# Performance work log

Measured on AMD Instinct MI355X. Metric: run time of the kernel, lower is better.

Reference implementation:

```python
import jax, jax.numpy as jnp
import numpy as np

EPS_BN = 1e-5
EPS_W = 1e-8


def setup_inputs() -> dict:
    key = jax.random.key(0)
    ks = jax.random.split(key, 6)
    B, N, S, D1, D2 = 8, 8192, 2048, 128, 256
    Cin = D1 + D2  # 384
    return {
        "points_position": jax.random.normal(ks[0], (B, 3, N), jnp.float32),
        "sampled_points_position": jax.random.normal(ks[1], (B, 3, S), jnp.float32),
        "skip_points_feature": jax.random.normal(ks[2], (B, D1, N), jnp.float32),
        "sampled_points_feature": jax.random.normal(ks[3], (B, D2, S), jnp.float32),
        "W1": jax.random.normal(ks[4], (256, Cin), jnp.float32) * 0.05,
        "b1": jnp.zeros((256,), jnp.float32),
        "g1": jnp.ones((256,), jnp.float32),
        "beta1": jnp.zeros((256,), jnp.float32),
        "W2": jax.random.normal(ks[5], (128, 256), jnp.float32) * 0.05,
        "b2": jnp.zeros((128,), jnp.float32),
        "g2": jnp.ones((128,), jnp.float32),
        "beta2": jnp.zeros((128,), jnp.float32),
    }


def _bn_relu(x, g, b):
    # train-mode BatchNorm1d over (batch, points) per channel, x: [B,N,C]
    mean = jnp.mean(x, axis=(0, 1), keepdims=True)
    var = jnp.mean(jnp.square(x - mean), axis=(0, 1), keepdims=True)  # biased var
    return jax.nn.relu((x - mean) * jax.lax.rsqrt(var + EPS_BN) * g + b)


def reference(points_position, sampled_points_position, skip_points_feature,
              sampled_points_feature, W1, b1, g1, beta1, W2, b2, g2, beta2):
    pos = points_position.transpose(0, 2, 1)            # [B,N,3]
    spos = sampled_points_position.transpose(0, 2, 1)   # [B,S,3]
    sfeat = sampled_points_feature.transpose(0, 2, 1)   # [B,S,D2]

    # squared pairwise distance [B,N,S]
    d = (jnp.sum(pos * pos, axis=-1, keepdims=True)
         - 2.0 * jnp.einsum("bnc,bsc->bns", pos, spos)
         + jnp.sum(spos * spos, axis=-1)[:, None, :])

    # 3 nearest neighbors (smallest distances)
    neg_d3, idx = jax.lax.top_k(-d, 3)                  # [B,N,3]
    d3 = -neg_d3
    w = 1.0 / (d3 + EPS_W)
    w = w / jnp.sum(w, axis=-1, keepdims=True)          # [B,N,3]

    gathered = jax.vmap(lambda f, i: f[i])(sfeat, idx)  # [B,N,3,D2]
    interp = jnp.einsum("bnk,bnkd->bnd", w, gathered)   # [B,N,D2]

    feat = jnp.concatenate([skip_points_feature.transpose(0, 2, 1), interp], axis=-1)  # [B,N,D1+D2]

    h = _bn_relu(jnp.einsum("bnc,oc->bno", feat, W1) + b1, g1, beta1)  # [B,N,256]
    h = _bn_relu(jnp.einsum("bnc,oc->bno", h, W2) + b2, g2, beta2)     # [B,N,128]
    return h.transpose(0, 2, 1)                          # [B,128,N]
```

## Files before the change

kernel.cpp:

```cpp
#include <hip/hip_runtime.h>

constexpr int BATCH = 8;
constexpr int NPT   = 8192;
constexpr int NSMP  = 2048;
constexpr int D1C   = 128;
constexpr int D2C   = 256;
constexpr int CIN   = 384;
constexpr int C1    = 256;
constexpr int C2    = 128;
constexpr int BN_TOTAL = BATCH * NPT;

constexpr int BM = 128, BK = 32;
constexpr int NRB = BN_TOTAL / BM;

typedef __bf16 bf16x8 __attribute__((ext_vector_type(8)));
typedef short  s16x8  __attribute__((ext_vector_type(8)));
typedef float  f32x4  __attribute__((ext_vector_type(4)));
typedef unsigned short u16x4 __attribute__((ext_vector_type(4)));

__device__ __forceinline__ unsigned short f2bf(float x) {
  unsigned u = __builtin_bit_cast(unsigned, x);
  u += 0x7fffu + ((u >> 16) & 1u);
  return (unsigned short)(u >> 16);
}
__device__ __forceinline__ float bf2f(unsigned short h) {
  return __builtin_bit_cast(float, (unsigned)h << 16);
}

__device__ __forceinline__ void gld_lds16(const void* g, void* l) {
  __builtin_amdgcn_global_load_lds(
      (const __attribute__((address_space(1))) void*)g,
      (__attribute__((address_space(3))) void*)l, 16, 0, 0);
}

constexpr int PT_T = (NSMP / 32) * (D2C / 32) * BATCH;
constexpr int PT_S = (NPT / 32) * (D1C / 32) * BATCH;
constexpr int PT_M = (C1 * CIN + 255) / 256;

__global__ __launch_bounds__(256) void prep_all(
    const float* __restrict__ sfeat, float* __restrict__ sfeatT,
    const float* __restrict__ skip, unsigned short* __restrict__ featB,
    const float* __restrict__ spos, float* __restrict__ sposI,
    float4* __restrict__ qs4,
    const float* __restrict__ W1, unsigned short* __restrict__ W1h,
    const float* __restrict__ W2, unsigned short* __restrict__ W2h,
    float* __restrict__ stats) {
  __shared__ float tile[32][33];
  int bid = blockIdx.x, tid = threadIdx.x;
  int tx = tid & 31, ty = tid >> 5;
  if (bid < PT_T) {
    int z = bid >> 9;
    int r = bid & 511;
    int c0 = (r & 63) * 32;
    int r0 = (r >> 6) * 32;
    const float* inb = sfeat + (size_t)z * D2C * NSMP;
    float* outb = sfeatT + (size_t)z * NSMP * D2C;
#pragma unroll
    for (int i = 0; i < 32; i += 8)
      tile[ty + i][tx] = inb[(size_t)(r0 + ty + i) * NSMP + c0 + tx];
    __syncthreads();
#pragma unroll
    for (int i = 0; i < 32; i += 8)
      outb[(size_t)(c0 + ty + i) * D2C + r0 + tx] = tile[tx][ty + i];
  } else if (bid < PT_T + PT_S) {
    int id = bid - PT_T;
    int z = id >> 10;
    int r = id & 1023;
    int n0 = (r & 255) * 32;
    int d0 = (r >> 8) * 32;
#pragma unroll
    for (int i = 0; i < 32; i += 8)
      tile[ty + i][tx] = skip[((size_t)z * D1C + d0 + ty + i) * NPT + n0 + tx];
    __syncthreads();
#pragma unroll
    for (int i = 0; i < 32; i += 8) {
      int n = n0 + ty + i;
      featB[((size_t)z * NPT + n) * CIN + d0 + tx] = f2bf(tile[tx][ty + i]);
    }
  } else {
    int g = (bid - PT_T - PT_S) * 256 + tid;
    if (g < 768) stats[g] = 0.f;
    if (g < C1 * CIN) W1h[g] = f2bf(W1[g]);
    if (g < C2 * C1)  W2h[g] = f2bf(W2[g]);
    if (g < BATCH * NSMP) {
      int b = g >> 11, s = g & (NSMP - 1);
      const float* sp = spos + (size_t)b * 3 * NSMP;
      float x = sp[s], y = sp[NSMP + s], z = sp[2 * NSMP + s];
      sposI[(size_t)g * 3 + 0] = x;
      sposI[(size_t)g * 3 + 1] = y;
      sposI[(size_t)g * 3 + 2] = z;
      qs4[g] = make_float4(-2.f * x, -2.f * y, -2.f * z,
                           fmaf(x, x, fmaf(y, y, z * z)));
    }
  }
}

constexpr int KWAVES = 8;
constexpr int SEGK = NSMP / KWAVES;
constexpr int PPB  = 128;

__device__ __forceinline__ void ins_med3(float kf, float& k0, float& k1,
                                         float& k2, float& k3) {
  float o0 = k0, o1 = k1, o2 = k2;
  k0 = fminf(kf, o0);
  k1 = __builtin_amdgcn_fmed3f(kf, o0, o1);
  k2 = __builtin_amdgcn_fmed3f(kf, o1, o2);
  k3 = __builtin_amdgcn_fmed3f(kf, o2, k3);
}

__device__ __forceinline__ bool dless(double d, int i, double D, int I) {
  return d < D || (d == D && i < I);
}
__device__ __forceinline__ void dins3(double d, int i,
                                      double& b0, double& b1, double& b2,
                                      int& i0, int& i1, int& i2) {
  if (dless(d, i, b2, i2)) {
    if (dless(d, i, b1, i1)) {
      b2 = b1; i2 = i1;
      if (dless(d, i, b0, i0)) { b1 = b0; i1 = i0; b0 = d; i0 = i; }
      else                     { b1 = d; i1 = i; }
    } else { b2 = d; i2 = i; }
  }
}

__global__ __launch_bounds__(512, 4) void knn_all(
    const float* __restrict__ pos,
    const float4* __restrict__ qs4g,
    const float* __restrict__ sposI,
    const float* __restrict__ sfeatT,
    unsigned short* __restrict__ featB) {
  __shared__ __align__(16) unsigned char smem[NSMP * 16];
  float4* qs  = (float4*)smem;
  float*  mkf = (float*)smem;
#define MKF(w, sl, m, l) mkf[(w) * 1024 + ((sl) * 2 + (m)) * 64 + (l)]
  __shared__ int   il[PPB][3];
  __shared__ float wl[PPB][3];
  __shared__ int   fl[PPB];
  __shared__ int   fcnt;

  int tid = threadIdx.x;
  int wave = tid >> 6, lane = tid & 63;
  int blk = blockIdx.x;
  int b = blk & 7;
  int n0 = (blk >> 3) * PPB;

  if (tid == 0) fcnt = 0;

  const float* pb = pos + (size_t)b * 3 * NPT;
  float px[2], py[2], pz[2], pp[2];
#pragma unroll
  for (int m = 0; m < 2; m++) {
    int n = n0 + (m << 6) + lane;
    px[m] = pb[n]; py[m] = pb[NPT + n]; pz[m] = pb[2 * NPT + n];
    pp[m] = fmaf(px[m], px[m], fmaf(py[m], py[m], pz[m] * pz[m]));
  }

  const float INF = __builtin_inff();
  float k0[2], k1[2], k2[2], k3[2];
#pragma unroll
  for (int m = 0; m < 2; m++) { k0[m] = INF; k1[m] = INF; k2[m] = INF; k3[m] = INF; }

  int s0 = wave * SEGK;
  const float4* qsrc = qs4g + (size_t)b * NSMP;
#pragma unroll
  for (int r = 0; r < 4; r++)
    gld_lds16(&qsrc[s0 + r * 64 + lane], &qs[s0 + r * 64]);
  __syncthreads();

#define KSTEP2(Q, SS)                                                        \
  {                                                                          \
    _Pragma("unroll")                                                        \
    for (int m_ = 0; m_ < 2; m_++) {                                         \
      float tt = (Q).w + pp[m_];       \
      float d_ = fmaf(px[m_], (Q).x,                                         \
                      fmaf(py[m_], (Q).y, fmaf(pz[m_], (Q).z, tt)));         \
      unsigned ki_ = (__builtin_bit_cast(unsigned, d_) & 0xFFFFF800u) |      \
                     (unsigned)(SS);                                         \
      ins_med3(__builtin_bit_cast(float, ki_), k0[m_], k1[m_], k2[m_], k3[m_]); \
    }                                                                        \
  }

  for (int t = 0; t < SEGK; t += 8) {
    float4 qv[8];
#pragma unroll
    for (int u = 0; u < 8; u++) qv[u] = qs[s0 + t + u];
#pragma unroll
    for (int u = 0; u < 8; u++) KSTEP2(qv[u], s0 + t + u)
  }
#undef KSTEP2

#pragma unroll
  for (int m = 0; m < 2; m++) {
    MKF(wave, 0, m, lane) = k0[m];
    MKF(wave, 1, m, lane) = k1[m];
    MKF(wave, 2, m, lane) = k2[m];
    MKF(wave, 3, m, lane) = k3[m];
  }
  __syncthreads();

  if (tid < PPB) {
    int pm = tid >> 6, pl = tid & 63;
    float K0 = INF, K1 = INF, K2 = INF, K3 = INF;
#pragma unroll
    for (int w = 0; w < KWAVES; w++)
#pragma unroll
      for (int sl = 0; sl < 4; sl++)
        ins_med3(MKF(w, sl, pm, pl), K0, K1, K2, K3);

    int I0 = (int)(__builtin_bit_cast(unsigned, K0) & 0x7FFu);
    int I1 = (int)(__builtin_bit_cast(unsigned, K1) & 0x7FFu);
    int I2 = (int)(__builtin_bit_cast(unsigned, K2) & 0x7FFu);
    float d2m = __builtin_bit_cast(float, __builtin_bit_cast(unsigned, K2) & 0xFFFFF800u);
    float d3m = __builtin_bit_cast(float, __builtin_bit_cast(unsigned, K3) & 0xFFFFF800u);
    bool flag = (d3m - d2m) < 2e-3f * fmaxf(d3m, 0.f) + 1e-5f;
    if (flag) {
      int slot = atomicAdd(&fcnt, 1);
      fl[slot] = tid;
    }
    int n = n0 + tid;
    const float* q = sposI + (size_t)b * 3 * NSMP;
    double pxd = (double)pb[n], pyd = (double)pb[NPT + n], pzd = (double)pb[2 * NPT + n];
    double dd[3]; int II[3] = {I0, I1, I2};
#pragma unroll
    for (int k = 0; k < 3; k++) {
      double dx = pxd - (double)q[3 * II[k]];
      double dy = pyd - (double)q[3 * II[k] + 1];
      double dz = pzd - (double)q[3 * II[k] + 2];
      dd[k] = dx * dx + dy * dy + dz * dz;
    }
    double w0 = 1.0 / (dd[0] + 1e-8);
    double w1 = 1.0 / (dd[1] + 1e-8);
    double w2 = 1.0 / (dd[2] + 1e-8);
    double inv = 1.0 / (w0 + w1 + w2);
    il[tid][0] = I0; il[tid][1] = I1; il[tid][2] = I2;
    wl[tid][0] = (float)(w0 * inv);
    wl[tid][1] = (float)(w1 * inv);
    wl[tid][2] = (float)(w2 * inv);
  }
  __syncthreads();

  int fc = fcnt;
  for (int t = wave; t < fc; t += KWAVES) {
    int P = fl[t];
    int n = n0 + P;
    double pxd = (double)pb[n], pyd = (double)pb[NPT + n], pzd = (double)pb[2 * NPT + n];
    const float* q = sposI + (size_t)b * 3 * NSMP;
    double b0 = 1e300, b1 = 1e300, b2 = 1e300;
    int i0 = 0x7FFFFFFF, i1 = 0x7FFFFFFF, i2 = 0x7FFFFFFF;
    for (int s = lane; s < NSMP; s += 64) {
      double dx = pxd - (double)q[3 * s];
      double dy = pyd - (double)q[3 * s + 1];
      double dz = pzd - (double)q[3 * s + 2];
      double d = dx * dx + dy * dy + dz * dz;
      dins3(d, s, b0, b1, b2, i0, i1, i2);
    }
#pragma unroll
    for (int m = 1; m < 64; m <<= 1) {
      double o0 = __shfl_xor(b0, m, 64), o1 = __shfl_xor(b1, m, 64), o2 = __shfl_xor(b2, m, 64);
      int    j0 = __shfl_xor(i0, m, 64), j1 = __shfl_xor(i1, m, 64), j2 = __shfl_xor(i2, m, 64);
      dins3(o0, j0, b0, b1, b2, i0, i1, i2);
      dins3(o1, j1, b0, b1, b2, i0, i1, i2);
      dins3(o2, j2, b0, b1, b2, i0, i1, i2);
    }
    if (lane == 0) {
      double w0 = 1.0 / (b0 + 1e-8);
      double w1 = 1.0 / (b1 + 1e-8);
      double w2 = 1.0 / (b2 + 1e-8);
      double inv = 1.0 / (w0 + w1 + w2);
      il[P][0] = i0; il[P][1] = i1; il[P][2] = i2;
      wl[P][0] = (float)(w0 * inv);
      wl[P][1] = (float)(w1 * inv);
      wl[P][2] = (float)(w2 * inv);
    }
  }
  __syncthreads();

  const float* base = sfeatT + (size_t)b * NSMP * D2C;
  for (int i = 0; i < 16; i++) {
    int P = (wave << 4) + i;
    int i0 = il[P][0], i1 = il[P][1], i2 = il[P][2];
    float w0 = wl[P][0], w1 = wl[P][1], w2 = wl[P][2];
    float4 v0 = *(const float4*)&base[(size_t)i0 * D2C + (lane << 2)];
    float4 v1 = *(const float4*)&base[(size_t)i1 * D2C + (lane << 2)];
    float4 v2 = *(const float4*)&base[(size_t)i2 * D2C + (lane << 2)];
    u16x4 o;
    o[0] = f2bf(w0 * v0.x + w1 * v1.x + w2 * v2.x);
    o[1] = f2bf(w0 * v0.y + w1 * v1.y + w2 * v2.y);
    o[2] = f2bf(w0 * v0.z + w1 * v1.z + w2 * v2.z);
    o[3] = f2bf(w0 * v0.w + w1 * v1.w + w2 * v2.w);
    *(u16x4*)&featB[((size_t)b * NPT + n0 + P) * CIN + D1C + (lane << 2)] = o;
  }
#undef MKF
}

__global__ __launch_bounds__(256) void gemm1_mw(
    const unsigned short* __restrict__ featB,
    const unsigned short* __restrict__ W1h,
    const float* __restrict__ bias,
    unsigned short* __restrict__ Y1,
    float* __restrict__ sum1,
    float* __restrict__ sumsq1) {
  __shared__ __align__(16) unsigned short As[BM * BK];
  __shared__ __align__(16) unsigned short Bs[BM * BK];
  int tid = threadIdx.x;
  int lane = tid & 63, w = tid >> 6;
  int wr = w >> 1, wc = w & 1;
  int m16 = lane & 15, quad = lane >> 4;
  int cb = blockIdx.x, rb = blockIdx.y;
  int row0 = rb * BM, col0 = cb * BM;
  int srow = lane >> 2, scol8 = (lane & 3) * 8;

  f32x4 acc[4][4];
#pragma unroll
  for (int j = 0; j < 4; j++) {
    float bj = bias[col0 + wc * 64 + j * 16 + m16];
#pragma unroll
    for (int i = 0; i < 4; i++) acc[i][j] = f32x4{bj, bj, bj, bj};
  }

  for (int k0 = 0; k0 < CIN; k0 += BK) {
#pragma unroll
    for (int kq = 0; kq < 2; kq++) {
      int ar = 32 * w + 16 * kq + srow;
      int lb = __builtin_amdgcn_readfirstlane((32 * w + 16 * kq) * BK);
      gld_lds16(&featB[(size_t)(row0 + ar) * CIN + k0 + scol8], &As[lb]);
      gld_lds16(&W1h[(size_t)(col0 + ar) * CIN + k0 + scol8], &Bs[lb]);
    }
    __syncthreads();

    bf16x8 a[4], bb[4];
#pragma unroll
    for (int i = 0; i < 4; i++)
      a[i] = __builtin_bit_cast(bf16x8,
          *(const s16x8*)&As[(wr * 64 + i * 16 + m16) * BK + quad * 8]);
#pragma unroll
    for (int j = 0; j < 4; j++)
      bb[j] = __builtin_bit_cast(bf16x8,
          *(const s16x8*)&Bs[(wc * 64 + j * 16 + m16) * BK + quad * 8]);
#pragma unroll
    for (int i = 0; i < 4; i++)
#pragma unroll
      for (int j = 0; j < 4; j++)
        acc[i][j] = __builtin_amdgcn_mfma_f32_16x16x32_bf16(a[i], bb[j], acc[i][j], 0, 0, 0);
    __syncthreads();
  }

#pragma unroll
  for (int j = 0; j < 4; j++) {
    int col = col0 + wc * 64 + j * 16 + m16;
    float s = 0.f, q = 0.f;
#pragma unroll
    for (int i = 0; i < 4; i++)
#pragma unroll
      for (int r = 0; r < 4; r++) {
        float v = acc[i][j][r];
        Y1[(size_t)(row0 + wr * 64 + i * 16 + quad * 4 + r) * C1 + col] = f2bf(v);
        s += v; q = fmaf(v, v, q);
      }
    s += __shfl_xor(s, 16, 64); s += __shfl_xor(s, 32, 64);
    q += __shfl_xor(q, 16, 64); q += __shfl_xor(q, 32, 64);
    if (quad == 0) {
      atomicAdd(&sum1[col], s);
      atomicAdd(&sumsq1[col], q);
    }
  }
}

__global__ __launch_bounds__(256) void gemm2_mw(
    const unsigned short* __restrict__ Y1,
    const float* __restrict__ g1, const float* __restrict__ beta1,
    const float* __restrict__ sum1, const float* __restrict__ sumsq1,
    const unsigned short* __restrict__ W2h,
    const float* __restrict__ bias,
    unsigned short* __restrict__ Y2,
    float* __restrict__ sum2, float* __restrict__ sumsq2) {
  __shared__ __align__(16) unsigned short As[BM * BK];
  __shared__ __align__(16) unsigned short Bs[BM * BK];
  __shared__ float scs[C1], shs[C1];
  int tid = threadIdx.x;
  int lane = tid & 63, w = tid >> 6;
  int wr = w >> 1, wc = w & 1;
  int m16 = lane & 15, quad = lane >> 4;
  int rb = blockIdx.x;
  int row0 = rb * BM, col0 = 0;
  int srow = lane >> 2, scol8 = (lane & 3) * 8;

  {
    const float invBN = 1.0f / (float)BN_TOTAL;
    float mean = sum1[tid] * invBN;
    float var = sumsq1[tid] * invBN - mean * mean;
    float sc = g1[tid] / sqrtf(var + 1e-5f);
    scs[tid] = sc;
    shs[tid] = beta1[tid] - mean * sc;
  }

  f32x4 acc[4][4];
#pragma unroll
  for (int j = 0; j < 4; j++) {
    float bj = bias[col0 + wc * 64 + j * 16 + m16];
#pragma unroll
    for (int i = 0; i < 4; i++) acc[i][j] = f32x4{bj, bj, bj, bj};
  }
  __syncthreads();

  for (int k0 = 0; k0 < C1; k0 += BK) {
#pragma unroll
    for (int kq = 0; kq < 2; kq++) {
      int ar = 32 * w + 16 * kq + srow;
      int lb = __builtin_amdgcn_readfirstlane((32 * w + 16 * kq) * BK);
      gld_lds16(&W2h[(size_t)(col0 + ar) * C1 + k0 + scol8], &Bs[lb]);
      s16x8 v = *(const s16x8*)&Y1[(size_t)(row0 + ar) * C1 + k0 + scol8];
      unsigned short ov[8];
#pragma unroll
      for (int e = 0; e < 8; e++) {
        float x = bf2f((unsigned short)v[e]);
        float y = fmaxf(fmaf(x, scs[k0 + scol8 + e], shs[k0 + scol8 + e]), 0.f);
        ov[e] = f2bf(y);
      }
      *(s16x8*)&As[ar * BK + scol8] = *(const s16x8*)ov;
    }
    __syncthreads();

    bf16x8 a[4], bb[4];
#pragma unroll
    for (int i = 0; i < 4; i++)
      a[i] = __builtin_bit_cast(bf16x8,
          *(const s16x8*)&As[(wr * 64 + i * 16 + m16) * BK + quad * 8]);
#pragma unroll
    for (int j = 0; j < 4; j++)
      bb[j] = __builtin_bit_cast(bf16x8,
          *(const s16x8*)&Bs[(wc * 64 + j * 16 + m16) * BK + quad * 8]);
#pragma unroll
    for (int i = 0; i < 4; i++)
#pragma unroll
      for (int j = 0; j < 4; j++)
        acc[i][j] = __builtin_amdgcn_mfma_f32_16x16x32_bf16(a[i], bb[j], acc[i][j], 0, 0, 0);
    __syncthreads();
  }

#pragma unroll
  for (int j = 0; j < 4; j++) {
    int col = col0 + wc * 64 + j * 16 + m16;
    float s = 0.f, q = 0.f;
#pragma unroll
    for (int i = 0; i < 4; i++)
#pragma unroll
      for (int r = 0; r < 4; r++) {
        float v = acc[i][j][r];
        Y2[(size_t)(row0 + wr * 64 + i * 16 + quad * 4 + r) * C2 + col] = f2bf(v);
        s += v; q = fmaf(v, v, q);
      }
    s += __shfl_xor(s, 16, 64); s += __shfl_xor(s, 32, 64);
    q += __shfl_xor(q, 16, 64); q += __shfl_xor(q, 32, 64);
    if (quad == 0) {
      atomicAdd(&sum2[col], s);
      atomicAdd(&sumsq2[col], q);
    }
  }
}

__global__ void final_kernel(const unsigned short* __restrict__ Y2,
                             const float* __restrict__ sum2,
                             const float* __restrict__ sumsq2,
                             const float* __restrict__ g2,
                             const float* __restrict__ beta2,
                             float* __restrict__ out) {
  __shared__ float tile[32][33];
  int b = blockIdx.z;
  int n0 = blockIdx.x * 32;
  int c0 = blockIdx.y * 32;
  int tx = threadIdx.x, ty = threadIdx.y;
  int c = c0 + tx;
  const float invBN = 1.0f / (float)BN_TOTAL;
  float mean = sum2[c] * invBN;
  float var = sumsq2[c] * invBN - mean * mean;
  float sc = g2[c] / sqrtf(var + 1e-5f);
  float sh = beta2[c] - mean * sc;
#pragma unroll
  for (int i = 0; i < 32; i += 8) {
    int n = n0 + ty + i;
    float v = bf2f(Y2[((size_t)b * NPT + n) * C2 + c0 + tx]);
    tile[ty + i][tx] = fmaxf(fmaf(v, sc, sh), 0.f);
  }
  __syncthreads();
#pragma unroll
  for (int i = 0; i < 32; i += 8) {
    int cc = c0 + ty + i;
    out[((size_t)b * C2 + cc) * NPT + n0 + tx] = tile[tx][ty + i];
  }
}

extern "C" void kernel_launch(void* const* d_in, const int* in_sizes, int n_in,
                              void* d_out, int out_size, void* d_ws, size_t ws_size,
                              hipStream_t stream) {
  (void)in_sizes; (void)n_in; (void)out_size; (void)ws_size;
  const float* pos   = (const float*)d_in[0];
  const float* spos  = (const float*)d_in[1];
  const float* skip  = (const float*)d_in[2];
  const float* sfeat = (const float*)d_in[3];
  const float* W1    = (const float*)d_in[4];
  const float* b1    = (const float*)d_in[5];
  const float* g1    = (const float*)d_in[6];
  const float* beta1 = (const float*)d_in[7];
  const float* W2    = (const float*)d_in[8];
  const float* b2    = (const float*)d_in[9];
  const float* g2    = (const float*)d_in[10];
  const float* beta2 = (const float*)d_in[11];
  float* out = (float*)d_out;

  float* ws = (float*)d_ws;
  size_t off = 0;
  float* sfeatT  = ws + off; off += (size_t)BATCH * NSMP * D2C;
  unsigned short* featB = (unsigned short*)(ws + off); off += (size_t)BN_TOTAL * CIN / 2;
  unsigned short* Y1    = (unsigned short*)(ws + off); off += (size_t)BN_TOTAL * C1 / 2;
  unsigned short* Y2    = (unsigned short*)(ws + off); off += (size_t)BN_TOTAL * C2 / 2;
  unsigned short* W1h   = (unsigned short*)(ws + off); off += (size_t)C1 * CIN / 2;
  unsigned short* W2h   = (unsigned short*)(ws + off); off += (size_t)C2 * C1 / 2;
  float* sposI   = ws + off; off += (size_t)BATCH * NSMP * 3;
  float4* qs4    = (float4*)(ws + off); off += (size_t)BATCH * NSMP * 4;
  float* stats   = ws + off; off += 1024;
  float* sum1   = stats;
  float* sumsq1 = stats + 256;
  float* sum2   = stats + 512;
  float* sumsq2 = stats + 640;

  prep_all<<<PT_T + PT_S + PT_M, 256, 0, stream>>>(
      sfeat, sfeatT, skip, featB, spos, sposI, qs4, W1, W1h, W2, W2h, stats);

  knn_all<<<BN_TOTAL / PPB, 512, 0, stream>>>(pos, qs4, sposI, sfeatT, featB);

  gemm1_mw<<<dim3(C1 / BM, NRB), 256, 0, stream>>>(
      featB, W1h, b1, Y1, sum1, sumsq1);

  gemm2_mw<<<NRB, 256, 0, stream>>>(
      Y1, g1, beta1, sum1, sumsq1, W2h, b2, Y2, sum2, sumsq2);

  final_kernel<<<dim3(NPT / 32, C2 / 32, BATCH), dim3(32, 8), 0, stream>>>(
      Y2, sum2, sumsq2, g2, beta2, out);
}
```

Baseline: 283.1 us.

## Widen gemm1 blocks to cover all output columns and pair knn gather points

gemm1 now launches one 512-thread block per 128-row tile that computes all 256 output channels, so each A tile of features is loaded once instead of once per column block. Rows stay with wr in 0..1 and columns with wc in 0..3. Separately, the knn interpolation loop handles two points per iteration to put more independent gather loads in flight. The cost is more LDS per block and half as many gemm1 blocks, which may lower occupancy.

New measurement: 284.0 us. About the same (+0.3%).

```diff
diff --git a/kernel.cpp b/kernel.cpp
--- a/kernel.cpp
+++ b/kernel.cpp
@@ -276,24 +276,34 @@
   __syncthreads();
 
   const float* base = sfeatT + (size_t)b * NSMP * D2C;
-  for (int i = 0; i < 16; i++) {
-    int P = (wave << 4) + i;
-    int i0 = il[P][0], i1 = il[P][1], i2 = il[P][2];
-    float w0 = wl[P][0], w1 = wl[P][1], w2 = wl[P][2];
-    float4 v0 = *(const float4*)&base[(size_t)i0 * D2C + (lane << 2)];
-    float4 v1 = *(const float4*)&base[(size_t)i1 * D2C + (lane << 2)];
-    float4 v2 = *(const float4*)&base[(size_t)i2 * D2C + (lane << 2)];
-    u16x4 o;
-    o[0] = f2bf(w0 * v0.x + w1 * v1.x + w2 * v2.x);
-    o[1] = f2bf(w0 * v0.y + w1 * v1.y + w2 * v2.y);
-    o[2] = f2bf(w0 * v0.z + w1 * v1.z + w2 * v2.z);
-    o[3] = f2bf(w0 * v0.w + w1 * v1.w + w2 * v2.w);
-    *(u16x4*)&featB[((size_t)b * NPT + n0 + P) * CIN + D1C + (lane << 2)] = o;
+  for (int i = 0; i < 16; i += 2) {
+    int P0 = (wave << 4) + i, P1 = P0 + 1;
+    int a0 = il[P0][0], a1 = il[P0][1], a2 = il[P0][2];
+    int c0 = il[P1][0], c1 = il[P1][1], c2 = il[P1][2];
+    float aw0 = wl[P0][0], aw1 = wl[P0][1], aw2 = wl[P0][2];
+    float cw0 = wl[P1][0], cw1 = wl[P1][1], cw2 = wl[P1][2];
+    float4 u0 = *(const float4*)&base[(size_t)a0 * D2C + (lane << 2)];
+    float4 u1 = *(const float4*)&base[(size_t)a1 * D2C + (lane << 2)];
+    float4 u2 = *(const float4*)&base[(size_t)a2 * D2C + (lane << 2)];
+    float4 v0 = *(const float4*)&base[(size_t)c0 * D2C + (lane << 2)];
+    float4 v1 = *(const float4*)&base[(size_t)c1 * D2C + (lane << 2)];
+    float4 v2 = *(const float4*)&base[(size_t)c2 * D2C + (lane << 2)];
+    u16x4 o0, o1;
+    o0[0] = f2bf(aw0 * u0.x + aw1 * u1.x + aw2 * u2.x);
+    o0[1] = f2bf(aw0 * u0.y + aw1 * u1.y + aw2 * u2.y);
+    o0[2] = f2bf(aw0 * u0.z + aw1 * u1.z + aw2 * u2.z);
+    o0[3] = f2bf(aw0 * u0.w + aw1 * u1.w + aw2 * u2.w);
+    o1[0] = f2bf(cw0 * v0.x + cw1 * v1.x + cw2 * v2.x);
+    o1[1] = f2bf(cw0 * v0.y + cw1 * v1.y + cw2 * v2.y);
+    o1[2] = f2bf(cw0 * v0.z + cw1 * v1.z + cw2 * v2.z);
+    o1[3] = f2bf(cw0 * v0.w + cw1 * v1.w + cw2 * v2.w);
+    *(u16x4*)&featB[((size_t)b * NPT + n0 + P0) * CIN + D1C + (lane << 2)] = o0;
+    *(u16x4*)&featB[((size_t)b * NPT + n0 + P1) * CIN + D1C + (lane << 2)] = o1;
   }
 #undef MKF
 }
 
-__global__ __launch_bounds__(256) void gemm1_mw(
+__global__ __launch_bounds__(512) void gemm1_mw(
     const unsigned short* __restrict__ featB,
     const unsigned short* __restrict__ W1h,
     const float* __restrict__ bias,
@@ -301,30 +311,34 @@
     float* __restrict__ sum1,
     float* __restrict__ sumsq1) {
   __shared__ __align__(16) unsigned short As[BM * BK];
-  __shared__ __align__(16) unsigned short Bs[BM * BK];
+  __shared__ __align__(16) unsigned short Bs[C1 * BK];
   int tid = threadIdx.x;
   int lane = tid & 63, w = tid >> 6;
-  int wr = w >> 1, wc = w & 1;
+  int wr = w >> 2, wc = w & 3;
   int m16 = lane & 15, quad = lane >> 4;
-  int cb = blockIdx.x, rb = blockIdx.y;
-  int row0 = rb * BM, col0 = cb * BM;
+  int rb = blockIdx.x;
+  int row0 = rb * BM;
   int srow = lane >> 2, scol8 = (lane & 3) * 8;
 
   f32x4 acc[4][4];
 #pragma unroll
   for (int j = 0; j < 4; j++) {
-    float bj = bias[col0 + wc * 64 + j * 16 + m16];
+    float bj = bias[wc * 64 + j * 16 + m16];
 #pragma unroll
     for (int i = 0; i < 4; i++) acc[i][j] = f32x4{bj, bj, bj, bj};
   }
 
   for (int k0 = 0; k0 < CIN; k0 += BK) {
-#pragma unroll
-    for (int kq = 0; kq < 2; kq++) {
-      int ar = 32 * w + 16 * kq + srow;
-      int lb = __builtin_amdgcn_readfirstlane((32 * w + 16 * kq) * BK);
-      gld_lds16(&featB[(size_t)(row0 + ar) * CIN + k0 + scol8], &As[lb]);
-      gld_lds16(&W1h[(size_t)(col0 + ar) * CIN + k0 + scol8], &Bs[lb]);
+    {
+      int lb = __builtin_amdgcn_readfirstlane((w * 16) * BK);
+      gld_lds16(&featB[(size_t)(row0 + w * 16 + srow) * CIN + k0 + scol8],
+                &As[lb]);
+    }
+#pragma unroll
+    for (int rr = 0; rr < 2; rr++) {
+      int lb = __builtin_amdgcn_readfirstlane((rr * 128 + w * 16) * BK);
+      gld_lds16(&W1h[(size_t)(rr * 128 + w * 16 + srow) * CIN + k0 + scol8],
+                &Bs[lb]);
     }
     __syncthreads();
 
@@ -347,7 +361,7 @@
 
 #pragma unroll
   for (int j = 0; j < 4; j++) {
-    int col = col0 + wc * 64 + j * 16 + m16;
+    int col = wc * 64 + j * 16 + m16;
     float s = 0.f, q = 0.f;
 #pragma unroll
     for (int i = 0; i < 4; i++)
@@ -529,8 +543,7 @@
 
   knn_all<<<BN_TOTAL / PPB, 512, 0, stream>>>(pos, qs4, sposI, sfeatT, featB);
 
-  gemm1_mw<<<dim3(C1 / BM, NRB), 256, 0, stream>>>(
-      featB, W1h, b1, Y1, sum1, sumsq1);
+  gemm1_mw<<<NRB, 512, 0, stream>>>(featB, W1h, b1, Y1, sum1, sumsq1);
 
   gemm2_mw<<<NRB, 256, 0, stream>>>(
       Y1, g1, beta1, sum1, sumsq1, W2h, b2, Y2, sum2, sumsq2);
```
